# Kernel optimization log

Measured on AMD Instinct MI355X. Metric: run time of the kernel, lower is better.

Reference implementation:

```python
import jax, jax.numpy as jnp
import numpy as np

B, S, F, E, D = 64, 64, 512, 1024, 1024

def setup_inputs() -> dict:
    key = jax.random.key(0)
    k1, k2, k3, k4, k5 = jax.random.split(key, 5)
    sen_emb = jax.random.normal(k1, (B, S, E), dtype=jnp.float32)
    features = jax.random.normal(k2, (B, F, D), dtype=jnp.float32)
    # lengths in [1, F] so softmax always has at least one valid element
    feature_lens = jax.random.randint(k3, (B,), 1, F + 1, dtype=jnp.int64)
    W = jax.random.normal(k4, (E + D,), dtype=jnp.float32) * (1.0 / np.sqrt(E + D))
    b = jax.random.normal(k5, (1,), dtype=jnp.float32) * 0.01
    return {"sen_emb": sen_emb, "features": features, "feature_lens": feature_lens, "W": W, "b": b}

def reference(sen_emb, features, feature_lens, W, b):
    E_ = sen_emb.shape[-1]
    W_e, W_f = W[:E_], W[E_:]
    # additive score decomposes: Linear(cat(e, f)) = e.W_e + f.W_f + b
    s_emb = jnp.einsum('bse,e->bs', sen_emb, W_e)          # [B, S]
    s_ftr = jnp.einsum('bfd,d->bf', features, W_f)          # [B, F]
    scores = s_emb[:, :, None] + s_ftr[:, None, :] + b[0]   # [B, S, F]
    valid = jnp.arange(features.shape[1])[None, :] < feature_lens[:, None]  # [B, F]
    neg = jnp.finfo(scores.dtype).min
    scores = jnp.where(valid[:, None, :], scores, neg)
    attn = jax.nn.softmax(scores, axis=-1)                  # [B, S, F]
    return jnp.einsum('bsf,bfd->bsd', attn, features)       # [B, S, D]
```

## Files before the change

kernel.cpp:

```cpp
#include <hip/hip_runtime.h>
#include <cfloat>

#define B_ 64
#define S_ 64
#define F_ 512
#define E_ 1024
#define D_ 1024

__global__ __launch_bounds__(256) void k_rowdot(const float* __restrict__ features,
                                                const float* __restrict__ W_f,
                                                const int* __restrict__ lens,
                                                float* __restrict__ s_ftr) {
    const int wave = threadIdx.x >> 6;
    const int lane = threadIdx.x & 63;
    const int row  = blockIdx.x * 4 + wave;
    const int b    = row >> 9;
    const int f    = row & (F_ - 1);
    if (f >= lens[b]) return;

    const float4* fp = reinterpret_cast<const float4*>(features + (size_t)row * D_);
    const float4* wp = reinterpret_cast<const float4*>(W_f);
    float acc = 0.f;
#pragma unroll
    for (int j = 0; j < 4; ++j) {
        const float4 v = fp[lane + 64 * j];
        const float4 w = wp[lane + 64 * j];
        acc = fmaf(v.x, w.x, acc);
        acc = fmaf(v.y, w.y, acc);
        acc = fmaf(v.z, w.z, acc);
        acc = fmaf(v.w, w.w, acc);
    }
#pragma unroll
    for (int off = 32; off; off >>= 1) acc += __shfl_xor(acc, off, 64);
    if (lane == 0) s_ftr[row] = acc;
}

__global__ __launch_bounds__(512) void k_softmax(const float* __restrict__ s_ftr,
                                                 const int* __restrict__ lens,
                                                 float* __restrict__ p) {
    __shared__ float red[8];
    const int b    = blockIdx.x;
    const int f    = threadIdx.x;
    const int len  = lens[b];
    const int wave = threadIdx.x >> 6;
    const int lane = threadIdx.x & 63;

    float v = (f < len) ? s_ftr[b * F_ + f] : -FLT_MAX;

    float m = v;
#pragma unroll
    for (int off = 32; off; off >>= 1) m = fmaxf(m, __shfl_xor(m, off, 64));
    if (lane == 0) red[wave] = m;
    __syncthreads();
    float m8 = red[0];
#pragma unroll
    for (int i = 1; i < 8; ++i) m8 = fmaxf(m8, red[i]);

    const float e = (f < len) ? __expf(v - m8) : 0.f;

    float s = e;
#pragma unroll
    for (int off = 32; off; off >>= 1) s += __shfl_xor(s, off, 64);
    __syncthreads();
    if (lane == 0) red[wave] = s;
    __syncthreads();
    float s8 = 0.f;
#pragma unroll
    for (int i = 0; i < 8; ++i) s8 += red[i];

    p[b * F_ + f] = e / s8;
}

__global__ __launch_bounds__(256) void k_ctx(const float* __restrict__ features,
                                             const float* __restrict__ p,
                                             const int* __restrict__ lens,
                                             float* __restrict__ out) {
    __shared__ float sp[F_];
    const int b   = blockIdx.y;
    const int d   = blockIdx.x * 256 + threadIdx.x;
    const int len = lens[b];

    for (int i = threadIdx.x; i < F_; i += 256) sp[i] = p[b * F_ + i];
    __syncthreads();

    const float* fb = features + (size_t)b * F_ * D_ + d;
    float acc = 0.f;
    int f = 0;
    for (; f + 8 <= len; f += 8) {
        const float a0 = fb[(size_t)(f + 0) * D_];
        const float a1 = fb[(size_t)(f + 1) * D_];
        const float a2 = fb[(size_t)(f + 2) * D_];
        const float a3 = fb[(size_t)(f + 3) * D_];
        const float a4 = fb[(size_t)(f + 4) * D_];
        const float a5 = fb[(size_t)(f + 5) * D_];
        const float a6 = fb[(size_t)(f + 6) * D_];
        const float a7 = fb[(size_t)(f + 7) * D_];
        acc = fmaf(sp[f + 0], a0, acc);
        acc = fmaf(sp[f + 1], a1, acc);
        acc = fmaf(sp[f + 2], a2, acc);
        acc = fmaf(sp[f + 3], a3, acc);
        acc = fmaf(sp[f + 4], a4, acc);
        acc = fmaf(sp[f + 5], a5, acc);
        acc = fmaf(sp[f + 6], a6, acc);
        acc = fmaf(sp[f + 7], a7, acc);
    }
    for (; f < len; ++f) acc = fmaf(sp[f], fb[(size_t)f * D_], acc);

    float* ob = out + (size_t)b * S_ * D_ + d;
#pragma unroll
    for (int s = 0; s < S_; ++s) ob[(size_t)s * D_] = acc;
}

extern "C" void kernel_launch(void* const* d_in, const int* in_sizes, int n_in,
                              void* d_out, int out_size, void* d_ws, size_t ws_size,
                              hipStream_t stream) {
    (void)in_sizes; (void)n_in; (void)out_size; (void)ws_size;
    const float* features = (const float*)d_in[1];
    const int*   lens     = (const int*)d_in[2];
    const float* W        = (const float*)d_in[3];
    float*       out      = (float*)d_out;

    float* s_ftr = (float*)d_ws;
    float* p     = s_ftr + B_ * F_;

    k_rowdot <<<dim3(B_ * F_ / 4), 256, 0, stream>>>(features, W + E_, lens, s_ftr);
    k_softmax<<<dim3(B_),          512, 0, stream>>>(s_ftr, lens, p);
    k_ctx    <<<dim3(D_ / 256, B_), 256, 0, stream>>>(features, p, lens, out);
}
```

Before: 212.4 us.

## Fuse softmax into split-F context kernel and parallelize output broadcast

Removes the standalone softmax kernel: each context block recomputes the per-batch softmax over the scores in shared memory. The context reduction is split over tiles of 32 feature rows, so the grid grows from 256 blocks to up to 1024, each reading float4-coalesced rows, and partial sums go to workspace. A new broadcast kernel sums the partials and writes the 64 identical output rows with float4 stores spread over 8 blocks per batch. The cost is redundant softmax work in every tile block and an extra round trip through workspace for the partials.

Result: no change. 209.5 us (-1.4%).

```diff
diff --git a/kernel.cpp b/kernel.cpp
--- a/kernel.cpp
+++ b/kernel.cpp
@@ -6,6 +6,8 @@
 #define F_ 512
 #define E_ 1024
 #define D_ 1024
+#define FT_ 32
+#define NT_ (F_ / FT_)
 
 __global__ __launch_bounds__(256) void k_rowdot(const float* __restrict__ features,
                                                 const float* __restrict__ W_f,
@@ -35,80 +37,75 @@
     if (lane == 0) s_ftr[row] = acc;
 }
 
-__global__ __launch_bounds__(512) void k_softmax(const float* __restrict__ s_ftr,
-                                                 const int* __restrict__ lens,
-                                                 float* __restrict__ p) {
-    __shared__ float red[8];
-    const int b    = blockIdx.x;
-    const int f    = threadIdx.x;
+__global__ __launch_bounds__(256) void k_ctx_part(const float* __restrict__ features,
+                                                  const float* __restrict__ s_ftr,
+                                                  const int* __restrict__ lens,
+                                                  float* __restrict__ part) {
+    const int b    = blockIdx.y;
+    const int tile = blockIdx.x;
     const int len  = lens[b];
-    const int wave = threadIdx.x >> 6;
-    const int lane = threadIdx.x & 63;
+    const int f0   = tile * FT_;
+    if (f0 >= len) return;
 
-    float v = (f < len) ? s_ftr[b * F_ + f] : -FLT_MAX;
+    __shared__ float sw[F_];
+    __shared__ float red_m[4], red_s[4];
+    const int t    = threadIdx.x;
+    const int wave = t >> 6;
+    const int lane = t & 63;
 
-    float m = v;
+    const float v0 = (t       < len) ? s_ftr[b * F_ + t]       : -FLT_MAX;
+    const float v1 = (t + 256 < len) ? s_ftr[b * F_ + t + 256] : -FLT_MAX;
+    float m = fmaxf(v0, v1);
 #pragma unroll
     for (int off = 32; off; off >>= 1) m = fmaxf(m, __shfl_xor(m, off, 64));
-    if (lane == 0) red[wave] = m;
+    if (lane == 0) red_m[wave] = m;
     __syncthreads();
-    float m8 = red[0];
-#pragma unroll
-    for (int i = 1; i < 8; ++i) m8 = fmaxf(m8, red[i]);
+    const float m4 = fmaxf(fmaxf(red_m[0], red_m[1]), fmaxf(red_m[2], red_m[3]));
 
-    const float e = (f < len) ? __expf(v - m8) : 0.f;
-
-    float s = e;
+    const float e0 = (t       < len) ? __expf(v0 - m4) : 0.f;
+    const float e1 = (t + 256 < len) ? __expf(v1 - m4) : 0.f;
+    float s = e0 + e1;
 #pragma unroll
     for (int off = 32; off; off >>= 1) s += __shfl_xor(s, off, 64);
+    if (lane == 0) red_s[wave] = s;
     __syncthreads();
-    if (lane == 0) red[wave] = s;
+    const float inv = 1.f / (red_s[0] + red_s[1] + red_s[2] + red_s[3]);
+    sw[t]       = e0 * inv;
+    sw[t + 256] = e1 * inv;
     __syncthreads();
-    float s8 = 0.f;
-#pragma unroll
-    for (int i = 0; i < 8; ++i) s8 += red[i];
 
-    p[b * F_ + f] = e / s8;
+    const float4* fb = reinterpret_cast<const float4*>(features + ((size_t)b * F_ + f0) * D_);
+    float4 acc = make_float4(0.f, 0.f, 0.f, 0.f);
+    const int nf = min(FT_, len - f0);
+    for (int f = 0; f < nf; ++f) {
+        const float  w = sw[f0 + f];
+        const float4 v = fb[f * 256 + t];
+        acc.x = fmaf(w, v.x, acc.x);
+        acc.y = fmaf(w, v.y, acc.y);
+        acc.z = fmaf(w, v.z, acc.z);
+        acc.w = fmaf(w, v.w, acc.w);
+    }
+    reinterpret_cast<float4*>(part)[((size_t)b * NT_ + tile) * 256 + t] = acc;
 }
 
-__global__ __launch_bounds__(256) void k_ctx(const float* __restrict__ features,
-                                             const float* __restrict__ p,
-                                             const int* __restrict__ lens,
-                                             float* __restrict__ out) {
-    __shared__ float sp[F_];
-    const int b   = blockIdx.y;
-    const int d   = blockIdx.x * 256 + threadIdx.x;
-    const int len = lens[b];
+__global__ __launch_bounds__(256) void k_bcast(const float* __restrict__ part,
+                                               const int* __restrict__ lens,
+                                               float* __restrict__ out) {
+    const int b  = blockIdx.y;
+    const int t  = threadIdx.x;
+    const int nt = min(NT_, (lens[b] + FT_ - 1) / FT_);
 
-    for (int i = threadIdx.x; i < F_; i += 256) sp[i] = p[b * F_ + i];
-    __syncthreads();
+    const float4* pp = reinterpret_cast<const float4*>(part) + (size_t)b * NT_ * 256 + t;
+    float4 acc = make_float4(0.f, 0.f, 0.f, 0.f);
+    for (int k = 0; k < nt; ++k) {
+        const float4 v = pp[(size_t)k * 256];
+        acc.x += v.x; acc.y += v.y; acc.z += v.z; acc.w += v.w;
+    }
 
-    const float* fb = features + (size_t)b * F_ * D_ + d;
-    float acc = 0.f;
-    int f = 0;
-    for (; f + 8 <= len; f += 8) {
-        const float a0 = fb[(size_t)(f + 0) * D_];
-        const float a1 = fb[(size_t)(f + 1) * D_];
-        const float a2 = fb[(size_t)(f + 2) * D_];
-        const float a3 = fb[(size_t)(f + 3) * D_];
-        const float a4 = fb[(size_t)(f + 4) * D_];
-        const float a5 = fb[(size_t)(f + 5) * D_];
-        const float a6 = fb[(size_t)(f + 6) * D_];
-        const float a7 = fb[(size_t)(f + 7) * D_];
-        acc = fmaf(sp[f + 0], a0, acc);
-        acc = fmaf(sp[f + 1], a1, acc);
-        acc = fmaf(sp[f + 2], a2, acc);
-        acc = fmaf(sp[f + 3], a3, acc);
-        acc = fmaf(sp[f + 4], a4, acc);
-        acc = fmaf(sp[f + 5], a5, acc);
-        acc = fmaf(sp[f + 6], a6, acc);
-        acc = fmaf(sp[f + 7], a7, acc);
-    }
-    for (; f < len; ++f) acc = fmaf(sp[f], fb[(size_t)f * D_], acc);
-
-    float* ob = out + (size_t)b * S_ * D_ + d;
+    const int s0 = blockIdx.x * 8;
+    float4* ob = reinterpret_cast<float4*>(out) + ((size_t)b * S_ + s0) * 256 + t;
 #pragma unroll
-    for (int s = 0; s < S_; ++s) ob[(size_t)s * D_] = acc;
+    for (int s = 0; s < 8; ++s) ob[(size_t)s * 256] = acc;
 }
 
 extern "C" void kernel_launch(void* const* d_in, const int* in_sizes, int n_in,
@@ -121,9 +118,9 @@
     float*       out      = (float*)d_out;
 
     float* s_ftr = (float*)d_ws;
-    float* p     = s_ftr + B_ * F_;
+    float* part  = s_ftr + B_ * F_;
 
-    k_rowdot <<<dim3(B_ * F_ / 4), 256, 0, stream>>>(features, W + E_, lens, s_ftr);
-    k_softmax<<<dim3(B_),          512, 0, stream>>>(s_ftr, lens, p);
-    k_ctx    <<<dim3(D_ / 256, B_), 256, 0, stream>>>(features, p, lens, out);
+    k_rowdot  <<<dim3(B_ * F_ / 4), 256, 0, stream>>>(features, W + E_, lens, s_ftr);
+    k_ctx_part<<<dim3(NT_, B_),     256, 0, stream>>>(features, s_ftr, lens, part);
+    k_bcast   <<<dim3(8, B_),       256, 0, stream>>>(part, lens, out);
 }
```
